# Performance work log

Hardware: AMD Instinct MI355X
Metric: run time of the kernel (lower is better)

The kernel has to match this reference:

```python
import jax, jax.numpy as jnp
import numpy as np

H, D = 8, 16          # heads, per-head dim (hidden_channels=128)
HID = H * D
N = 200000            # movie nodes
E = 500000            # edges per metapath relation
IN = 256              # input feature dim
CLS = 3               # output classes


def setup_inputs() -> dict:
    key = jax.random.key(0)
    ks = jax.random.split(key, 13)
    return {
        "x_movie": jax.random.normal(ks[0], (N, IN), jnp.float32),
        "W_proj": jax.random.normal(ks[1], (IN, HID), jnp.float32) * 0.05,
        "b_proj": jnp.zeros((HID,), jnp.float32),
        "att_src0": jax.random.normal(ks[2], (H, D), jnp.float32) * 0.1,
        "att_dst0": jax.random.normal(ks[3], (H, D), jnp.float32) * 0.1,
        "att_src1": jax.random.normal(ks[4], (H, D), jnp.float32) * 0.1,
        "att_dst1": jax.random.normal(ks[5], (H, D), jnp.float32) * 0.1,
        "q": jax.random.normal(ks[6], (HID,), jnp.float32) * 0.1,
        "k_w": jax.random.normal(ks[7], (HID, HID), jnp.float32) * 0.05,
        "k_b": jnp.zeros((HID,), jnp.float32),
        "lin_w": jax.random.normal(ks[8], (HID, CLS), jnp.float32) * 0.05,
        "lin_b": jnp.zeros((CLS,), jnp.float32),
        "e0_src": jax.random.randint(ks[9], (E,), 0, N, jnp.int32),
        "e0_dst": jax.random.randint(ks[10], (E,), 0, N, jnp.int32),
        "e1_src": jax.random.randint(ks[11], (E,), 0, N, jnp.int32),
        "e1_dst": jax.random.randint(ks[12], (E,), 0, N, jnp.int32),
    }


def _han_rel(h, att_s, att_d, src, dst, n):
    # h: [N, H, D]; GAT-style per-relation attention with segment softmax over dst
    a_s = jnp.sum(h * att_s, axis=-1)                      # [N, H]
    a_d = jnp.sum(h * att_d, axis=-1)                      # [N, H]
    alpha = jax.nn.leaky_relu(a_s[src] + a_d[dst], 0.2)    # [E, H]
    m = jax.ops.segment_max(alpha, dst, num_segments=n)    # per-dst max
    ex = jnp.exp(alpha - m[dst])
    den = jax.ops.segment_sum(ex, dst, num_segments=n)
    w = ex / (den[dst] + 1e-16)                            # edge softmax (PyG eps)
    msg = (h[src] * w[:, :, None]).reshape(-1, HID)        # [E, HID]
    return jax.nn.relu(jax.ops.segment_sum(msg, dst, num_segments=n))


def reference(x_movie, W_proj, b_proj, att_src0, att_dst0, att_src1, att_dst1,
              q, k_w, k_b, lin_w, lin_b, e0_src, e0_dst, e1_src, e1_dst):
    # node-type projection (HANConv.proj), dropout omitted (eval mode)
    h = (x_movie @ W_proj + b_proj).reshape(-1, H, D)      # [N, H, D]
    out0 = _han_rel(h, att_src0, att_dst0, e0_src, e0_dst, N)  # [N, HID]
    out1 = _han_rel(h, att_src1, att_dst1, e1_src, e1_dst, N)
    # semantic-level attention (HANConv.group)
    outs = jnp.stack([out0, out1])                         # [M=2, N, HID]
    score = jnp.sum(jnp.tanh(outs @ k_w + k_b).mean(axis=1) * q, axis=-1)  # [M]
    beta = jax.nn.softmax(score)
    fused = jnp.einsum('m,mnf->nf', beta, outs)            # [N, HID]
    return fused @ lin_w + lin_b                           # [N, CLS]
```

## Files before the change

### kernel.cpp

```cpp
#include <hip/hip_runtime.h>


typedef __attribute__((ext_vector_type(8))) short bf16x8;
typedef __attribute__((ext_vector_type(4))) float f32x4;
typedef __attribute__((ext_vector_type(8))) unsigned short ushort8;

__device__ __forceinline__ unsigned short f2b(float f) {
  union { float f; unsigned u; } v; v.f = f;
  unsigned r = v.u + 0x7fffu + ((v.u >> 16) & 1u);
  return (unsigned short)(r >> 16);
}
__device__ __forceinline__ float b2f(unsigned short u) {
  union { unsigned u; float f; } v; v.u = ((unsigned)u) << 16;
  return v.f;
}
__device__ __forceinline__ float fast_tanh(float x) {
  x = fminf(fmaxf(x, -15.f), 15.f);
  float t = __expf(2.f * x);
  return 1.f - 2.f / (t + 1.f);
}
__device__ __forceinline__ void gload_lds16(const void* g, void* l) {
  __builtin_amdgcn_global_load_lds(
      (const __attribute__((address_space(1))) unsigned int*)g,
      (__attribute__((address_space(3))) unsigned int*)l, 16, 0, 0);
}

__global__ __launch_bounds__(256) void prep_lite(
    const int* __restrict__ e0d, const int* __restrict__ e1d,
    int* __restrict__ deg, int ne, int n,
    const float* __restrict__ Wp, const float* __restrict__ kwm,
    unsigned short* __restrict__ Wpf, unsigned short* __restrict__ Kwf) {
  const int tid = threadIdx.x;
  int b = blockIdx.x;
  const int cb = (2 * ne + 255) >> 8;
  if (b < cb) {
    int e = b * 256 + tid;
    if (e < ne) atomicAdd(&deg[e0d[e]], 1);
    else if (e < 2 * ne) atomicAdd(&deg[n + e1d[e - ne]], 1);
    return;
  }
  b -= cb;
  int t = b * 256 + tid;
  const float* W; unsigned short* Wf; int idx;
  if (t < 4096) { W = Wp; Wf = Wpf; idx = t; }
  else if (t < 6144) { W = kwm; Wf = Kwf; idx = t - 4096; }
  else return;
  int lane = idx & 63, nt = (idx >> 6) & 7, kt = idx >> 9;
  int c = lane & 15, ks = lane >> 4;
  int kbase = kt * 32 + ks * 8;
  int col = nt * 16 + c;
  ushort8 o;
#pragma unroll
  for (int j = 0; j < 8; ++j) o[j] = f2b(W[(size_t)(kbase + j) * 128 + col]);
  *(ushort8*)(Wf + (size_t)idx * 8) = o;
}

__global__ __launch_bounds__(256) void proj_mfma(
    const float* __restrict__ X, const unsigned short* __restrict__ Wf,
    const float* __restrict__ bias,
    const float* __restrict__ as0v, const float* __restrict__ ad0v,
    const float* __restrict__ as1v, const float* __restrict__ ad1v,
    unsigned short* __restrict__ Hb, float* __restrict__ preb, int n) {
  __shared__ float buf[2][4096];
  const int tid = threadIdx.x;
  const int wid = tid >> 6, lane = tid & 63;
  const int wm = wid >> 1, wn = wid & 1;
  const int row0 = blockIdx.x * 64;
  const int r = lane & 15, ks = lane >> 4;

  f32x4 acc[2][4] = {};
  const unsigned short* bptr = Wf + ((size_t)(wn * 4) * 64 + lane) * 8;

#define STAGE(b, s)                                                            \
  {                                                                            \
    _Pragma("unroll")                                                          \
    for (int i = 0; i < 4; ++i) {                                              \
      int rloc = wid * 16 + i * 4 + ks;                                        \
      int grow = row0 + rloc;                                                  \
      grow = grow < n ? grow : n - 1;                                          \
      const float* src =                                                       \
          X + (size_t)grow * 256 + (s) * 64 + ((r ^ (rloc & 7)) << 2);         \
      gload_lds16(src, &buf[b][(wid * 16 + i * 4) * 64]);                      \
    }                                                                          \
  }

#define COMPUTE(b, s)                                                          \
  {                                                                            \
    _Pragma("unroll")                                                          \
    for (int kt = 0; kt < 2; ++kt) {                                           \
      bf16x8 a[2], bb[4];                                                      \
      _Pragma("unroll")                                                        \
      for (int mi = 0; mi < 2; ++mi) {                                         \
        int rr = wm * 32 + mi * 16 + r;                                        \
        const float* lrow = &buf[b][rr * 64];                                  \
        int c0 = kt * 8 + ks * 2;                                              \
        int sw = rr & 7;                                                       \
        float4 f0 = *(const float4*)(lrow + ((c0 ^ sw) * 4));                  \
        float4 f1 = *(const float4*)(lrow + (((c0 + 1) ^ sw) * 4));            \
        bf16x8 v;                                                              \
        v[0] = (short)f2b(f0.x); v[1] = (short)f2b(f0.y);                      \
        v[2] = (short)f2b(f0.z); v[3] = (short)f2b(f0.w);                      \
        v[4] = (short)f2b(f1.x); v[5] = (short)f2b(f1.y);                      \
        v[6] = (short)f2b(f1.z); v[7] = (short)f2b(f1.w);                      \
        a[mi] = v;                                                             \
      }                                                                        \
      _Pragma("unroll")                                                        \
      for (int ni = 0; ni < 4; ++ni)                                           \
        bb[ni] = *(const bf16x8*)(bptr + (((size_t)(s) * 2 + kt) * 8 + ni) * 512); \
      _Pragma("unroll")                                                        \
      for (int mi = 0; mi < 2; ++mi)                                           \
        _Pragma("unroll")                                                      \
        for (int ni = 0; ni < 4; ++ni)                                         \
          acc[mi][ni] = __builtin_amdgcn_mfma_f32_16x16x32_bf16(               \
              a[mi], bb[ni], acc[mi][ni], 0, 0, 0);                            \
    }                                                                          \
  }

  STAGE(0, 0);
  __syncthreads();
  STAGE(1, 1); COMPUTE(0, 0); __syncthreads();
  STAGE(0, 2); COMPUTE(1, 1); __syncthreads();
  STAGE(1, 3); COMPUTE(0, 2); __syncthreads();
  COMPUTE(1, 3);
  __syncthreads();
#undef STAGE
#undef COMPUTE

  unsigned short* ct = (unsigned short*)&buf[0][0];
#pragma unroll
  for (int ni = 0; ni < 4; ++ni) {
    const int col = wn * 64 + ni * 16 + r;
    const float bv = bias[col];
#pragma unroll
    for (int mi = 0; mi < 2; ++mi)
#pragma unroll
      for (int i = 0; i < 4; ++i)
        ct[(wm * 32 + mi * 16 + ks * 4 + i) * 136 + col] = f2b(acc[mi][ni][i] + bv);
  }
  __syncthreads();

  {
    int row = tid >> 2, qq = tid & 3;
    int grow = row0 + row;
    if (grow < n) {
      ushort8* dst = (ushort8*)(Hb + (size_t)grow * 128 + qq * 32);
#pragma unroll
      for (int j = 0; j < 4; ++j) dst[j] = *(ushort8*)&ct[row * 136 + qq * 32 + j * 8];
    }
  }

  const size_t n8 = (size_t)n * 8;
  for (int rh = tid; rh < 512; rh += 256) {
    int row = rh >> 3, head = rh & 7;
    int node = row0 + row;
    if (node < n) {
      float hv[16];
#pragma unroll
      for (int j = 0; j < 16; ++j) hv[j] = b2f(ct[row * 136 + head * 16 + j]);
      float s0 = 0, d0 = 0, s1 = 0, d1 = 0;
      const float* p0 = as0v + head * 16;
      const float* p1 = ad0v + head * 16;
      const float* p2 = as1v + head * 16;
      const float* p3 = ad1v + head * 16;
#pragma unroll
      for (int j = 0; j < 16; ++j) {
        float v = hv[j];
        s0 += v * p0[j]; d0 += v * p1[j];
        s1 += v * p2[j]; d1 += v * p3[j];
      }
      size_t idx = (size_t)node * 8 + head;
      preb[idx] = s0;
      preb[n8 + idx] = d0;
      preb[2 * n8 + idx] = s1;
      preb[3 * n8 + idx] = d1;
    }
  }
}

__global__ __launch_bounds__(256) void scan1_kernel(
    const int* __restrict__ deg, int* __restrict__ pre, int* __restrict__ bsum, int m) {
  __shared__ int sd[256];
  int t = threadIdx.x;
  int base = blockIdx.x * 2048 + t * 8;
  int v[8], sum = 0;
#pragma unroll
  for (int j = 0; j < 8; ++j) {
    v[j] = (base + j < m) ? deg[base + j] : 0;
    sum += v[j];
  }
  sd[t] = sum;
  __syncthreads();
  for (int off = 1; off < 256; off <<= 1) {
    int x = (t >= off) ? sd[t - off] : 0;
    __syncthreads();
    if (t >= off) sd[t] += x;
    __syncthreads();
  }
  if (t == 255) bsum[blockIdx.x] = sd[255];
  int run = sd[t] - sum;
#pragma unroll
  for (int j = 0; j < 8; ++j) {
    if (base + j < m) pre[base + j] = run;
    run += v[j];
  }
}

__global__ __launch_bounds__(256) void scan2_kernel(int* __restrict__ bsum, int nb) {
  __shared__ int sd[256];
  int t = threadIdx.x;
  int v = (t < nb) ? bsum[t] : 0;
  sd[t] = v;
  __syncthreads();
  for (int off = 1; off < 256; off <<= 1) {
    int x = (t >= off) ? sd[t - off] : 0;
    __syncthreads();
    if (t >= off) sd[t] += x;
    __syncthreads();
  }
  if (t < nb) bsum[t] = sd[t] - v;
}

__global__ void scan3_kernel(int* __restrict__ pre, const int* __restrict__ bsum, int m, int total) {
  int i = blockIdx.x * 256 + threadIdx.x;
  if (i < m) pre[i] += bsum[i >> 11];
  if (i == m) pre[m] = total;
}

__global__ void fill2_kernel(const int* __restrict__ e0s, const int* __restrict__ e0d,
                             const int* __restrict__ e1s, const int* __restrict__ e1d,
                             const int* __restrict__ pre, int* __restrict__ cur,
                             int* __restrict__ csr, int ne, int n) {
  int e = blockIdx.x * 256 + threadIdx.x;
  int s, idx;
  if (e < ne) { idx = e0d[e]; s = e0s[e]; }
  else if (e < 2 * ne) { idx = n + e1d[e - ne]; s = e1s[e - ne]; }
  else return;
  int slot = pre[idx] + atomicAdd(&cur[idx], 1);
  csr[slot] = s;
}

__global__ __launch_bounds__(256) void agg2_kernel(
    const int* __restrict__ pre, const int* __restrict__ csr,
    const unsigned short* __restrict__ Hb, const float* __restrict__ preb,
    unsigned short* __restrict__ outb, int n) {
  int rel = blockIdx.y;
  int gid = blockIdx.x * 256 + threadIdx.x;
  int node = gid >> 3;
  int lane = gid & 7;
  if (node >= n) return;
  const size_t n8 = (size_t)n * 8;
  const float* a_s = preb + (size_t)(2 * rel) * n8;
  const float* a_d = preb + (size_t)(2 * rel + 1) * n8;
  int beg = pre[rel * n + node], end = pre[rel * n + node + 1];
  float ad = a_d[(size_t)node * 8 + lane];
  float s = 0.f;
  float acc[16] = {};
  int e = beg;
  for (; e + 1 < end; e += 2) {
    int s0 = csr[e], s1 = csr[e + 1];
    float al0 = a_s[(size_t)s0 * 8 + lane] + ad;
    float al1 = a_s[(size_t)s1 * 8 + lane] + ad;
    const ushort8* h0p = (const ushort8*)(Hb + (size_t)s0 * 128 + lane * 16);
    const ushort8* h1p = (const ushort8*)(Hb + (size_t)s1 * 128 + lane * 16);
    ushort8 h0a = h0p[0], h0b = h0p[1];
    ushort8 h1a = h1p[0], h1b = h1p[1];
    al0 = (al0 >= 0.f) ? al0 : 0.2f * al0;
    al1 = (al1 >= 0.f) ? al1 : 0.2f * al1;
    float p0 = __expf(al0), p1 = __expf(al1);
    s += p0 + p1;
#pragma unroll
    for (int j = 0; j < 8; ++j) {
      acc[j]     += p0 * b2f(h0a[j]) + p1 * b2f(h1a[j]);
      acc[8 + j] += p0 * b2f(h0b[j]) + p1 * b2f(h1b[j]);
    }
  }
  if (e < end) {
    int s0 = csr[e];
    float al0 = a_s[(size_t)s0 * 8 + lane] + ad;
    const ushort8* h0p = (const ushort8*)(Hb + (size_t)s0 * 128 + lane * 16);
    ushort8 h0a = h0p[0], h0b = h0p[1];
    al0 = (al0 >= 0.f) ? al0 : 0.2f * al0;
    float p0 = __expf(al0);
    s += p0;
#pragma unroll
    for (int j = 0; j < 8; ++j) {
      acc[j]     += p0 * b2f(h0a[j]);
      acc[8 + j] += p0 * b2f(h0b[j]);
    }
  }
  float inv = 1.f / (s + 1e-16f);
  ushort8 o0, o1;
#pragma unroll
  for (int j = 0; j < 8; ++j) {
    o0[j] = f2b(fmaxf(acc[j] * inv, 0.f));
    o1[j] = f2b(fmaxf(acc[8 + j] * inv, 0.f));
  }
  ushort8* dst = (ushort8*)(outb + (size_t)rel * n * 128 + (size_t)node * 128 + lane * 16);
  dst[0] = o0;
  dst[1] = o1;
}

__global__ __launch_bounds__(256) void score2_mfma(
    const unsigned short* __restrict__ outb, const unsigned short* __restrict__ Kf,
    const float* __restrict__ kb, const float* __restrict__ q,
    const float* __restrict__ lw, float* __restrict__ pout,
    float* __restrict__ sb, int n) {
  __shared__ unsigned short at[16384];
  __shared__ float red[256];
  const int rel = blockIdx.y;
  const unsigned short* A = outb + (size_t)rel * n * 128;
  const int tid = threadIdx.x;
  const int wid = tid >> 6, lane = tid & 63;
  const int wm = wid >> 1, wn = wid & 1;
  const int row0 = blockIdx.x * 128;
  const int r = lane & 15, ks = lane >> 4;

  {
    unsigned short* dstbase = at + wid * 4096;
#pragma unroll
    for (int i = 0; i < 8; ++i) {
      int chunk = i * 64 + lane;
      int row = wid * 32 + (chunk >> 4);
      int c = chunk & 15;
      int grow = row0 + row;
      grow = grow < n ? grow : n - 1;
      const unsigned short* src = A + (size_t)grow * 128 + ((c ^ (row & 7)) * 8);
      gload_lds16(src, dstbase + i * 512);
    }
  }
  __syncthreads();

  f32x4 acc[4][4] = {};
  const unsigned short* bptr = Kf + ((size_t)(wn * 4) * 64 + lane) * 8;
#pragma unroll
  for (int kt = 0; kt < 4; ++kt) {
    bf16x8 a[4], b[4];
#pragma unroll
    for (int mi = 0; mi < 4; ++mi) {
      int row = wm * 64 + mi * 16 + r;
      a[mi] = *(const bf16x8*)&at[row * 128 + (((kt * 4 + ks) ^ (row & 7)) * 8)];
    }
#pragma unroll
    for (int ni = 0; ni < 4; ++ni)
      b[ni] = *(const bf16x8*)(bptr + ((size_t)kt * 8 + ni) * 512);
#pragma unroll
    for (int mi = 0; mi < 4; ++mi)
#pragma unroll
      for (int ni = 0; ni < 4; ++ni)
        acc[mi][ni] = __builtin_amdgcn_mfma_f32_16x16x32_bf16(a[mi], b[ni], acc[mi][ni], 0, 0, 0);
  }

  if (tid < 128) {
    int node = row0 + tid;
    if (node < n) {
      float p0 = 0.f, p1 = 0.f, p2 = 0.f;
      int s = tid & 7;
#pragma unroll
      for (int c = 0; c < 16; ++c) {
        const unsigned short* rp = &at[tid * 128 + ((c ^ s) * 8)];
#pragma unroll
        for (int j = 0; j < 8; ++j) {
          float v = b2f(rp[j]);
          const float* w = lw + (size_t)(c * 8 + j) * 3;
          p0 += v * w[0]; p1 += v * w[1]; p2 += v * w[2];
        }
      }
      float4 o = make_float4(p0, p1, p2, 0.f);
      *(float4*)(pout + (size_t)node * 8 + rel * 4) = o;
    }
  }

  float part = 0.f;
#pragma unroll
  for (int ni = 0; ni < 4; ++ni) {
    const int col = wn * 64 + ni * 16 + r;
    const float kbv = kb[col], qv = q[col];
#pragma unroll
    for (int mi = 0; mi < 4; ++mi) {
#pragma unroll
      for (int i = 0; i < 4; ++i) {
        int row = row0 + wm * 64 + mi * 16 + ks * 4 + i;
        if (row < n) part += fast_tanh(acc[mi][ni][i] + kbv) * qv;
      }
    }
  }
  red[tid] = part;
  __syncthreads();
  for (int off = 128; off > 0; off >>= 1) {
    if (tid < off) red[tid] += red[tid + off];
    __syncthreads();
  }
  if (tid == 0) atomicAdd(&sb[rel], red[0]);
}

__global__ void beta_kernel(float* __restrict__ sb, float invn) {
  if (threadIdx.x == 0 && blockIdx.x == 0) {
    float s0 = sb[0] * invn, s1 = sb[1] * invn;
    float m = fmaxf(s0, s1);
    float e0 = __expf(s0 - m), e1 = __expf(s1 - m);
    float d = e0 + e1;
    sb[2] = e0 / d;
    sb[3] = e1 / d;
  }
}

__global__ __launch_bounds__(256) void final2_kernel(
    const float* __restrict__ pout, const float* __restrict__ sb,
    const float* __restrict__ lb, float* __restrict__ out, int n) {
  int node = blockIdx.x * 256 + threadIdx.x;
  if (node >= n) return;
  float b0 = sb[2], b1 = sb[3];
  const float4* p = (const float4*)(pout + (size_t)node * 8);
  float4 pa = p[0], pb = p[1];
  float* d = out + (size_t)node * 3;
  d[0] = b0 * pa.x + b1 * pb.x + lb[0];
  d[1] = b0 * pa.y + b1 * pb.y + lb[1];
  d[2] = b0 * pa.z + b1 * pb.z + lb[2];
}

extern "C" void kernel_launch(void* const* d_in, const int* in_sizes, int n_in,
                              void* d_out, int out_size, void* d_ws, size_t ws_size,
                              hipStream_t stream) {
  const float* x   = (const float*)d_in[0];
  const float* Wp  = (const float*)d_in[1];
  const float* bp  = (const float*)d_in[2];
  const float* as0 = (const float*)d_in[3];
  const float* ad0 = (const float*)d_in[4];
  const float* as1 = (const float*)d_in[5];
  const float* ad1 = (const float*)d_in[6];
  const float* q   = (const float*)d_in[7];
  const float* kw  = (const float*)d_in[8];
  const float* kb  = (const float*)d_in[9];
  const float* lw  = (const float*)d_in[10];
  const float* lb  = (const float*)d_in[11];
  const int* e0s = (const int*)d_in[12];
  const int* e0d = (const int*)d_in[13];
  const int* e1s = (const int*)d_in[14];
  const int* e1d = (const int*)d_in[15];
  const int n  = in_sizes[0] / 256;
  const int ne = in_sizes[12];
  float* out = (float*)d_out;

  char* ws = (char*)d_ws;
  size_t off = 0;
  auto alloc = [&](size_t b) -> char* {
    char* p = ws + off;
    off = (off + b + 255) & ~(size_t)255;
    return p;
  };
  unsigned short* h    = (unsigned short*)alloc((size_t)n * 128 * 2);
  unsigned short* outb = (unsigned short*)alloc((size_t)2 * n * 128 * 2);
  float* preb = (float*)alloc((size_t)4 * n * 8 * 4);
  float* pout = (float*)alloc((size_t)n * 8 * 4);
  int* pre    = (int*)alloc((size_t)(2 * n + 1) * 4);
  int* csr    = (int*)alloc((size_t)2 * ne * 4);
  int* deg    = (int*)alloc(((size_t)4 * n + 4) * 4);
  int* cur    = deg + 2 * n;
  float* sb   = (float*)(deg + 4 * n);
  int* bsum   = (int*)alloc(256 * 4);
  unsigned short* Wpf = (unsigned short*)alloc((size_t)4096 * 8 * 2);
  unsigned short* Kwf = (unsigned short*)alloc((size_t)2048 * 8 * 2);

  const int m = 2 * n;
  const int nblk_scan = (m + 2047) / 2048;
  const int cnt_blks = (2 * ne + 255) / 256;

  hipMemsetAsync(deg, 0, ((size_t)4 * n + 4) * 4, stream);
  hipLaunchKernelGGL(prep_lite, dim3(cnt_blks + 24), dim3(256), 0, stream,
                     e0d, e1d, deg, ne, n, Wp, kw, Wpf, Kwf);

  const int gproj = (n + 63) / 64;
  hipLaunchKernelGGL(proj_mfma, dim3(gproj), dim3(256), 0, stream,
                     x, Wpf, bp, as0, ad0, as1, ad1, h, preb, n);

  hipLaunchKernelGGL(scan1_kernel, dim3(nblk_scan), dim3(256), 0, stream, deg, pre, bsum, m);
  hipLaunchKernelGGL(scan2_kernel, dim3(1), dim3(256), 0, stream, bsum, nblk_scan);
  hipLaunchKernelGGL(scan3_kernel, dim3((m + 1 + 255) / 256), dim3(256), 0, stream,
                     pre, bsum, m, 2 * ne);
  hipLaunchKernelGGL(fill2_kernel, dim3((2 * ne + 255) / 256), dim3(256), 0, stream,
                     e0s, e0d, e1s, e1d, pre, cur, csr, ne, n);
  hipLaunchKernelGGL(agg2_kernel, dim3((n * 8 + 255) / 256, 2), dim3(256), 0, stream,
                     pre, csr, h, preb, outb, n);

  hipLaunchKernelGGL(score2_mfma, dim3((n + 127) / 128, 2), dim3(256), 0, stream,
                     outb, Kwf, kb, q, lw, pout, sb, n);
  hipLaunchKernelGGL(beta_kernel, dim3(1), dim3(64), 0, stream, sb, 1.0f / n);
  hipLaunchKernelGGL(final2_kernel, dim3((n + 255) / 256), dim3(256), 0, stream,
                     pout, sb, lb, out, n);
}
```

Baseline: 335.8 us.

## Fuse edge aggregation into semantic score MFMA kernel via LDS tile

Merges the per-relation attention aggregation kernel with the semantic-score MFMA kernel. Each block aggregates 128 destination nodes directly into a swizzled LDS tile, then runs the k_w GEMM, tanh and reductions from LDS. This removes the round trip of the 2×N×128 bf16 intermediate through global memory and one kernel launch. In exchange, each block now carries both the irregular gather phase and the MFMA phase in sequence, with 4 nodes per thread group, which may lower the parallelism available to hide gather latency.

```diff
diff --git a/kernel.cpp b/kernel.cpp
--- a/kernel.cpp
+++ b/kernel.cpp
@@ -239,97 +239,84 @@
   csr[slot] = s;
 }
 
-__global__ __launch_bounds__(256) void agg2_kernel(
+__global__ __launch_bounds__(256) void aggscore_mfma(
     const int* __restrict__ pre, const int* __restrict__ csr,
     const unsigned short* __restrict__ Hb, const float* __restrict__ preb,
-    unsigned short* __restrict__ outb, int n) {
-  int rel = blockIdx.y;
-  int gid = blockIdx.x * 256 + threadIdx.x;
-  int node = gid >> 3;
-  int lane = gid & 7;
-  if (node >= n) return;
+    const unsigned short* __restrict__ Kf, const float* __restrict__ kb,
+    const float* __restrict__ q, const float* __restrict__ lw,
+    float* __restrict__ pout, float* __restrict__ sb, int n) {
+  __shared__ unsigned short at[16384];
+  __shared__ float red[256];
+  const int rel = blockIdx.y;
+  const int tid = threadIdx.x;
+  const int row0 = blockIdx.x * 128;
   const size_t n8 = (size_t)n * 8;
   const float* a_s = preb + (size_t)(2 * rel) * n8;
   const float* a_d = preb + (size_t)(2 * rel + 1) * n8;
-  int beg = pre[rel * n + node], end = pre[rel * n + node + 1];
-  float ad = a_d[(size_t)node * 8 + lane];
-  float s = 0.f;
-  float acc[16] = {};
-  int e = beg;
-  for (; e + 1 < end; e += 2) {
-    int s0 = csr[e], s1 = csr[e + 1];
-    float al0 = a_s[(size_t)s0 * 8 + lane] + ad;
-    float al1 = a_s[(size_t)s1 * 8 + lane] + ad;
-    const ushort8* h0p = (const ushort8*)(Hb + (size_t)s0 * 128 + lane * 16);
-    const ushort8* h1p = (const ushort8*)(Hb + (size_t)s1 * 128 + lane * 16);
-    ushort8 h0a = h0p[0], h0b = h0p[1];
-    ushort8 h1a = h1p[0], h1b = h1p[1];
-    al0 = (al0 >= 0.f) ? al0 : 0.2f * al0;
-    al1 = (al1 >= 0.f) ? al1 : 0.2f * al1;
-    float p0 = __expf(al0), p1 = __expf(al1);
-    s += p0 + p1;
-#pragma unroll
-    for (int j = 0; j < 8; ++j) {
-      acc[j]     += p0 * b2f(h0a[j]) + p1 * b2f(h1a[j]);
-      acc[8 + j] += p0 * b2f(h0b[j]) + p1 * b2f(h1b[j]);
-    }
-  }
-  if (e < end) {
-    int s0 = csr[e];
-    float al0 = a_s[(size_t)s0 * 8 + lane] + ad;
-    const ushort8* h0p = (const ushort8*)(Hb + (size_t)s0 * 128 + lane * 16);
-    ushort8 h0a = h0p[0], h0b = h0p[1];
-    al0 = (al0 >= 0.f) ? al0 : 0.2f * al0;
-    float p0 = __expf(al0);
-    s += p0;
-#pragma unroll
-    for (int j = 0; j < 8; ++j) {
-      acc[j]     += p0 * b2f(h0a[j]);
-      acc[8 + j] += p0 * b2f(h0b[j]);
-    }
-  }
-  float inv = 1.f / (s + 1e-16f);
-  ushort8 o0, o1;
-#pragma unroll
-  for (int j = 0; j < 8; ++j) {
-    o0[j] = f2b(fmaxf(acc[j] * inv, 0.f));
-    o1[j] = f2b(fmaxf(acc[8 + j] * inv, 0.f));
-  }
-  ushort8* dst = (ushort8*)(outb + (size_t)rel * n * 128 + (size_t)node * 128 + lane * 16);
-  dst[0] = o0;
-  dst[1] = o1;
-}
-
-__global__ __launch_bounds__(256) void score2_mfma(
-    const unsigned short* __restrict__ outb, const unsigned short* __restrict__ Kf,
-    const float* __restrict__ kb, const float* __restrict__ q,
-    const float* __restrict__ lw, float* __restrict__ pout,
-    float* __restrict__ sb, int n) {
-  __shared__ unsigned short at[16384];
-  __shared__ float red[256];
-  const int rel = blockIdx.y;
-  const unsigned short* A = outb + (size_t)rel * n * 128;
-  const int tid = threadIdx.x;
+
+  {
+    const int lane8 = tid & 7;
+    const int nsub = tid >> 3;
+#pragma unroll
+    for (int it = 0; it < 4; ++it) {
+      int row = it * 32 + nsub;
+      int node = row0 + row;
+      float s = 0.f;
+      float acc[16] = {};
+      if (node < n) {
+        int beg = pre[rel * n + node], end = pre[rel * n + node + 1];
+        float ad = a_d[(size_t)node * 8 + lane8];
+        int e = beg;
+        for (; e + 1 < end; e += 2) {
+          int s0 = csr[e], s1 = csr[e + 1];
+          float al0 = a_s[(size_t)s0 * 8 + lane8] + ad;
+          float al1 = a_s[(size_t)s1 * 8 + lane8] + ad;
+          const ushort8* h0p = (const ushort8*)(Hb + (size_t)s0 * 128 + lane8 * 16);
+          const ushort8* h1p = (const ushort8*)(Hb + (size_t)s1 * 128 + lane8 * 16);
+          ushort8 h0a = h0p[0], h0b = h0p[1];
+          ushort8 h1a = h1p[0], h1b = h1p[1];
+          al0 = (al0 >= 0.f) ? al0 : 0.2f * al0;
+          al1 = (al1 >= 0.f) ? al1 : 0.2f * al1;
+          float p0 = __expf(al0), p1 = __expf(al1);
+          s += p0 + p1;
+#pragma unroll
+          for (int j = 0; j < 8; ++j) {
+            acc[j]     += p0 * b2f(h0a[j]) + p1 * b2f(h1a[j]);
+            acc[8 + j] += p0 * b2f(h0b[j]) + p1 * b2f(h1b[j]);
+          }
+        }
+        if (e < end) {
+          int s0 = csr[e];
+          float al0 = a_s[(size_t)s0 * 8 + lane8] + ad;
+          const ushort8* h0p = (const ushort8*)(Hb + (size_t)s0 * 128 + lane8 * 16);
+          ushort8 h0a = h0p[0], h0b = h0p[1];
+          al0 = (al0 >= 0.f) ? al0 : 0.2f * al0;
+          float p0 = __expf(al0);
+          s += p0;
+#pragma unroll
+          for (int j = 0; j < 8; ++j) {
+            acc[j]     += p0 * b2f(h0a[j]);
+            acc[8 + j] += p0 * b2f(h0b[j]);
+          }
+        }
+      }
+      float inv = 1.f / (s + 1e-16f);
+      ushort8 o0, o1;
+#pragma unroll
+      for (int j = 0; j < 8; ++j) {
+        o0[j] = f2b(fmaxf(acc[j] * inv, 0.f));
+        o1[j] = f2b(fmaxf(acc[8 + j] * inv, 0.f));
+      }
+      int sw = row & 7;
+      *(ushort8*)&at[row * 128 + (((lane8 * 2) ^ sw) * 8)] = o0;
+      *(ushort8*)&at[row * 128 + (((lane8 * 2 + 1) ^ sw) * 8)] = o1;
+    }
+  }
+  __syncthreads();
+
   const int wid = tid >> 6, lane = tid & 63;
   const int wm = wid >> 1, wn = wid & 1;
-  const int row0 = blockIdx.x * 128;
   const int r = lane & 15, ks = lane >> 4;
-
-  {
-    unsigned short* dstbase = at + wid * 4096;
-#pragma unroll
-    for (int i = 0; i < 8; ++i) {
-      int chunk = i * 64 + lane;
-      int row = wid * 32 + (chunk >> 4);
-      int c = chunk & 15;
-      int grow = row0 + row;
-      grow = grow < n ? grow : n - 1;
-      const unsigned short* src = A + (size_t)grow * 128 + ((c ^ (row & 7)) * 8);
-      gload_lds16(src, dstbase + i * 512);
-    }
-  }
-  __syncthreads();
-
   f32x4 acc[4][4] = {};
   const unsigned short* bptr = Kf + ((size_t)(wn * 4) * 64 + lane) * 8;
 #pragma unroll
@@ -449,7 +436,6 @@
     return p;
   };
   unsigned short* h    = (unsigned short*)alloc((size_t)n * 128 * 2);
-  unsigned short* outb = (unsigned short*)alloc((size_t)2 * n * 128 * 2);
   float* preb = (float*)alloc((size_t)4 * n * 8 * 4);
   float* pout = (float*)alloc((size_t)n * 8 * 4);
   int* pre    = (int*)alloc((size_t)(2 * n + 1) * 4);
@@ -479,11 +465,9 @@
                      pre, bsum, m, 2 * ne);
   hipLaunchKernelGGL(fill2_kernel, dim3((2 * ne + 255) / 256), dim3(256), 0, stream,
                      e0s, e0d, e1s, e1d, pre, cur, csr, ne, n);
-  hipLaunchKernelGGL(agg2_kernel, dim3((n * 8 + 255) / 256, 2), dim3(256), 0, stream,
-                     pre, csr, h, preb, outb, n);
-
-  hipLaunchKernelGGL(score2_mfma, dim3((n + 127) / 128, 2), dim3(256), 0, stream,
-                     outb, Kwf, kb, q, lw, pout, sb, n);
+
+  hipLaunchKernelGGL(aggscore_mfma, dim3((n + 127) / 128, 2), dim3(256), 0, stream,
+                     pre, csr, h, preb, Kwf, kb, q, lw, pout, sb, n);
   hipLaunchKernelGGL(beta_kernel, dim3(1), dim3(64), 0, stream, sb, 1.0f / n);
   hipLaunchKernelGGL(final2_kernel, dim3((n + 255) / 256), dim3(256), 0, stream,
                      pout, sb, lb, out, n);
```

After: 320.8 us. 4.5% less time.
